# Performance work log

Measured on AMD Instinct MI355X. Metric: run time of the kernel, lower is better.

## Reference

```python
import jax, jax.numpy as jnp
import numpy as np

BF16_MIN = -3.3895313892515355e+38  # torch.finfo(torch.bfloat16).min
B, S, D = 2, 2048, 2048
H, KVH = 32, 8
HD = D // H  # 64


def setup_inputs() -> dict:
    key = jax.random.key(0)
    ks = jax.random.split(key, 7)
    scale = 0.02
    x = jax.random.normal(ks[0], (B, S, D), dtype=jnp.float32)
    # rotary tables as in llama2.c: theta = 10000^{-2i/hd}
    inv_freq = 1.0 / (10000.0 ** (np.arange(0, HD, 2, dtype=np.float32) / HD))
    t = np.arange(S, dtype=np.float32)
    freqs = np.outer(t, inv_freq)  # (S, HD//2)
    freqs_cos = jnp.asarray(np.cos(freqs))
    freqs_sin = jnp.asarray(np.sin(freqs))
    wq = jax.random.normal(ks[1], (H * HD, D), dtype=jnp.float32) * scale
    wk = jax.random.normal(ks[2], (KVH * HD, D), dtype=jnp.float32) * scale
    wv = jax.random.normal(ks[3], (KVH * HD, D), dtype=jnp.float32) * scale
    wo = jax.random.normal(ks[4], (D, H * HD), dtype=jnp.float32) * scale
    attn_mask = jnp.ones((B, S), dtype=jnp.int32)
    return {"x": x, "freqs_cos": freqs_cos, "freqs_sin": freqs_sin,
            "wq": wq, "wk": wk, "wv": wv, "wo": wo, "attn_mask": attn_mask}


def _rope(x, cos, sin):
    # x: (b, s, h, hd) -> split into interleaved real/imag pairs
    b, s, h, hd = x.shape
    xr = x[..., 0::2]
    xi = x[..., 1::2]
    cos = cos[None, :, None, :]  # (1, s, 1, hd//2)
    sin = sin[None, :, None, :]
    out_r = xr * cos - xi * sin
    out_i = xr * sin + xi * cos
    return jnp.stack([out_r, out_i], axis=-1).reshape(b, s, h, hd)


def reference(x, freqs_cos, freqs_sin, wq, wk, wv, wo, attn_mask):
    b, s, d = x.shape
    n_rep = H // KVH
    xq = jnp.einsum('bsd,ed->bse', x, wq).reshape(b, s, H, HD)
    xk = jnp.einsum('bsd,ed->bse', x, wk).reshape(b, s, KVH, HD)
    xv = jnp.einsum('bsd,ed->bse', x, wv).reshape(b, s, KVH, HD)
    xq = _rope(xq, freqs_cos, freqs_sin)
    xk = _rope(xk, freqs_cos, freqs_sin)
    # GQA repeat_kv: (b, s, kvh, hd) -> (b, s, kvh*n_rep, hd)
    xk = jnp.repeat(xk, n_rep, axis=2)
    xv = jnp.repeat(xv, n_rep, axis=2)
    # (b, h, s, hd)
    xq = xq.transpose(0, 2, 1, 3)
    xk = xk.transpose(0, 2, 1, 3)
    xv = xv.transpose(0, 2, 1, 3)
    causal = jnp.triu(jnp.full((s, s), BF16_MIN, dtype=x.dtype), k=1)[None, None]
    pad = jnp.where(attn_mask[:, None, :] == 0, BF16_MIN, 0.0).astype(x.dtype)  # (b,1,s) -> broadcast over query
    combined = causal + pad[:, None, :, :]  # (b,1,s,s)
    scores = jnp.einsum('bhqd,bhkd->bhqk', xq, xk) / np.sqrt(HD).astype(x.dtype)
    scores = jax.nn.softmax(scores + combined, axis=-1)
    out = jnp.einsum('bhqk,bhkd->bhqd', scores, xv)
    out = out.transpose(0, 2, 1, 3).reshape(b, s, H * HD)
    return jnp.einsum('bse,de->bsd', out, wo)
```

## Files before the change

### kernel.cpp

```cpp
#include <hip/hip_runtime.h>

typedef unsigned short u16;
typedef unsigned int u32;
typedef __attribute__((ext_vector_type(8))) short bf16x8;
typedef __attribute__((ext_vector_type(4))) float f32x4;

#define S_LEN 2048
#define QKV_N 3072
#define CEXP 0.18033688011f
#define M32C 5.77078016f

__device__ __forceinline__ u16 f2bf(float f) {
  u32 u = __builtin_bit_cast(u32, f);
  u32 r = (u + 0x7FFFu + ((u >> 16) & 1u)) >> 16;
  return (u16)r;
}
__device__ __forceinline__ float b2f(u16 h) {
  u32 u = ((u32)h) << 16;
  return __builtin_bit_cast(float, u);
}
__device__ __forceinline__ u32 pack_bf(float lo, float hi) {
  u32 a = __builtin_bit_cast(u32, lo) + 0x8000u;
  u32 b = __builtin_bit_cast(u32, hi) + 0x8000u;
  return __builtin_amdgcn_perm(b, a, 0x07060302u);
}
__device__ __forceinline__ void gload16(const void* g, void* l) {
  __builtin_amdgcn_global_load_lds(
      (const __attribute__((address_space(1))) u32*)g,
      (__attribute__((address_space(3))) u32*)l, 16, 0, 0);
}

__global__ void cast_bf16_x4(const float* __restrict__ s, u16* __restrict__ d) {
  int i = blockIdx.x * 256 + threadIdx.x;
  float4 v = ((const float4*)s)[i];
  u32 lo = (u32)f2bf(v.x) | ((u32)f2bf(v.y) << 16);
  u32 hi = (u32)f2bf(v.z) | ((u32)f2bf(v.w) << 16);
  ((uint2*)d)[i] = make_uint2(lo, hi);
}

template <int BN, int WM, int WN, int OUT_BF16>
__global__ __launch_bounds__(512, 2) void gemm_bt2(const u16* __restrict__ A,
                                                   const u16* __restrict__ B,
                                                   void* __restrict__ Cv,
                                                   int K, int ldc, int nbx) {
  constexpr int BM = 256;
  constexpr int MR = BM / WM / 16;
  constexpr int NR = BN / WN / 16;
  constexpr int MR2 = MR / 2, NR2 = NR / 2;
  constexpr int AR = BM / 64, BR = BN / 64;
  __shared__ u16 As0[BM * 64], As1[BM * 64];
  __shared__ u16 Bs0[BN * 64], Bs1[BN * 64];

  const int tid = threadIdx.x;
  const int lane = tid & 63, w = tid >> 6;
  const int wm = w / WN, wn = w % WN;
  const int g = lane >> 4, r16 = lane & 15;
  const int swz = r16 & 7;

  const int nwg = gridDim.x;
  const int q = nwg >> 3, r = nwg & 7;
  const int xcd = blockIdx.x & 7, off = blockIdx.x >> 3;
  const int wg = (xcd < r ? xcd * (q + 1) : r * (q + 1) + (xcd - r) * q) + off;
  const int m0 = (wg / nbx) * BM, n0 = (wg % nbx) * BN;

  const int rowi = tid >> 3;
  const int scol = ((tid & 7) ^ (rowi & 7)) * 8;
  const u16* Ag0 = A + (size_t)(m0 + rowi) * K + scol;
  const u16* Bg0 = B + (size_t)(n0 + rowi) * K + scol;

  f32x4 acc[MR][NR];
#pragma unroll
  for (int mi = 0; mi < MR; ++mi)
#pragma unroll
    for (int ni = 0; ni < NR; ++ni) acc[mi][ni] = f32x4{0.f, 0.f, 0.f, 0.f};

  auto stage = [&](int kb, u16* Ad, u16* Bd) {
#pragma unroll
    for (int rr = 0; rr < AR; ++rr)
      gload16(Ag0 + (size_t)rr * 64 * K + kb, Ad + rr * 4096 + tid * 8);
#pragma unroll
    for (int rr = 0; rr < BR; ++rr)
      gload16(Bg0 + (size_t)rr * 64 * K + kb, Bd + rr * 4096 + tid * 8);
  };

  auto compute = [&](const u16* Asrc, const u16* Bsrc) {
    bf16x8 ac[MR2][2], bc[NR][2];
    const u16* Aw = Asrc + (wm * MR * 16 + r16) * 64;
    const u16* Bw = Bsrc + (wn * NR * 16 + r16) * 64;
#pragma unroll
    for (int mi = 0; mi < MR2; ++mi)
#pragma unroll
      for (int kk = 0; kk < 2; ++kk)
        ac[mi][kk] = *(const bf16x8*)(Aw + mi * 1024 + ((kk * 4 + g) ^ swz) * 8);
#pragma unroll
    for (int ni = 0; ni < NR2; ++ni)
#pragma unroll
      for (int kk = 0; kk < 2; ++kk)
        bc[ni][kk] = *(const bf16x8*)(Bw + ni * 1024 + ((kk * 4 + g) ^ swz) * 8);
    __builtin_amdgcn_s_setprio(1);
#pragma unroll
    for (int mi = 0; mi < MR2; ++mi)
#pragma unroll
      for (int ni = 0; ni < NR2; ++ni)
#pragma unroll
        for (int kk = 0; kk < 2; ++kk)
          acc[mi][ni] = __builtin_amdgcn_mfma_f32_16x16x32_bf16(
              ac[mi][kk], bc[ni][kk], acc[mi][ni], 0, 0, 0);
    __builtin_amdgcn_s_setprio(0);
#pragma unroll
    for (int ni = NR2; ni < NR; ++ni)
#pragma unroll
      for (int kk = 0; kk < 2; ++kk)
        bc[ni][kk] = *(const bf16x8*)(Bw + ni * 1024 + ((kk * 4 + g) ^ swz) * 8);
    __builtin_amdgcn_s_setprio(1);
#pragma unroll
    for (int mi = 0; mi < MR2; ++mi)
#pragma unroll
      for (int ni = NR2; ni < NR; ++ni)
#pragma unroll
        for (int kk = 0; kk < 2; ++kk)
          acc[mi][ni] = __builtin_amdgcn_mfma_f32_16x16x32_bf16(
              ac[mi][kk], bc[ni][kk], acc[mi][ni], 0, 0, 0);
    __builtin_amdgcn_s_setprio(0);
#pragma unroll
    for (int mi = 0; mi < MR2; ++mi)
#pragma unroll
      for (int kk = 0; kk < 2; ++kk)
        ac[mi][kk] =
            *(const bf16x8*)(Aw + (MR2 + mi) * 1024 + ((kk * 4 + g) ^ swz) * 8);
    __builtin_amdgcn_s_setprio(1);
#pragma unroll
    for (int mi = 0; mi < MR2; ++mi)
#pragma unroll
      for (int ni = NR2; ni < NR; ++ni)
#pragma unroll
        for (int kk = 0; kk < 2; ++kk)
          acc[MR2 + mi][ni] = __builtin_amdgcn_mfma_f32_16x16x32_bf16(
              ac[mi][kk], bc[ni][kk], acc[MR2 + mi][ni], 0, 0, 0);
    __builtin_amdgcn_s_setprio(0);
    __builtin_amdgcn_s_setprio(1);
#pragma unroll
    for (int mi = 0; mi < MR2; ++mi)
#pragma unroll
      for (int ni = 0; ni < NR2; ++ni)
#pragma unroll
        for (int kk = 0; kk < 2; ++kk)
          acc[MR2 + mi][ni] = __builtin_amdgcn_mfma_f32_16x16x32_bf16(
              ac[mi][kk], bc[ni][kk], acc[MR2 + mi][ni], 0, 0, 0);
    __builtin_amdgcn_s_setprio(0);
  };

  const int NT = K >> 6;
  stage(0, As0, Bs0);
  __syncthreads();
  for (int t = 0; t < NT; t += 2) {
    if (t + 1 < NT) stage((t + 1) * 64, As1, Bs1);
    compute(As0, Bs0);
    __syncthreads();
    if (t + 2 < NT) stage((t + 2) * 64, As0, Bs0);
    compute(As1, Bs1);
    __syncthreads();
  }

#pragma unroll
  for (int mi = 0; mi < MR; ++mi)
#pragma unroll
    for (int ni = 0; ni < NR; ++ni) {
      int row = m0 + wm * MR * 16 + mi * 16 + g * 4;
      int col = n0 + wn * NR * 16 + ni * 16 + r16;
#pragma unroll
      for (int j = 0; j < 4; ++j) {
        if (OUT_BF16)
          ((u16*)Cv)[(size_t)(row + j) * ldc + col] = f2bf(acc[mi][ni][j]);
        else
          ((float*)Cv)[(size_t)(row + j) * ldc + col] = acc[mi][ni][j];
      }
    }
}

__global__ void rope_k(u16* qkv, const float* __restrict__ fc,
                       const float* __restrict__ fs) {
  const int p = blockIdx.x * 256 + threadIdx.x;
  const int row = blockIdx.y;
  const int s = row & (S_LEN - 1);
  const int i = p & 31;
  const float c = fc[s * 32 + i], sn = fs[s * 32 + i];
  u32 v = *(const u32*)&qkv[(size_t)row * QKV_N + 2 * p];
  float xr = b2f((u16)(v & 0xffffu)), xi = b2f((u16)(v >> 16));
  float orr = xr * c - xi * sn;
  float oi = xr * sn + xi * c;
  u32 o = (u32)f2bf(orr) | ((u32)f2bf(oi) << 16);
  *(u32*)&qkv[(size_t)row * QKV_N + 2 * p] = o;
}

__global__ void vtrans_k(const u16* __restrict__ qkv, u16* __restrict__ vt) {
  int i = blockIdx.x * 256 + threadIdx.x;
  int s = i & 2047;
  int d = (i >> 11) & 63;
  int bk = i >> 17;
  int b = bk >> 3, kv = bk & 7;
  vt[i] = qkv[(size_t)(b * 2048 + s) * QKV_N + 2560 + kv * 64 + d];
}

__global__ __launch_bounds__(256, 3) void attn_fwd(const u16* __restrict__ qkv,
                                                   const u16* __restrict__ vt,
                                                   u16* __restrict__ aout) {
  __shared__ u16 Ks[2][64 * 64];
  __shared__ u16 Vs[2][64 * 64];
  __shared__ u16 Ps[4][16 * 64];

  const int bh = blockIdx.x;
  const int qt = 15 - (int)blockIdx.y;
  const int b = bh >> 5, h = bh & 31, kvh = h >> 2;
  const int tid = threadIdx.x;
  const int w = tid >> 6, lane = tid & 63;
  const int g = lane >> 4, r16 = lane & 15;
  const int q0w = qt * 128 + w * 32;

  const u16* kbase = qkv + (size_t)b * S_LEN * QKV_N + 2048 + kvh * 64;
  const u16* vbase = vt + (size_t)(b * 8 + kvh) * 64 * S_LEN;

  const int srow = lane >> 3;
  const int scol = ((lane & 7) * 8) ^ (srow * 8);
  const int swz = (r16 & 7) * 8;

  bf16x8 qf[2][2];
#pragma unroll
  for (int qs = 0; qs < 2; ++qs) {
    const u16* qrow =
        qkv + (size_t)(b * S_LEN + q0w + qs * 16 + r16) * QKV_N + h * 64;
#pragma unroll
    for (int dh = 0; dh < 2; ++dh)
      qf[qs][dh] = *(const bf16x8*)(qrow + dh * 32 + g * 8);
  }

  f32x4 oacc[2][4];
#pragma unroll
  for (int qs = 0; qs < 2; ++qs)
#pragma unroll
    for (int dt = 0; dt < 4; ++dt) oacc[qs][dt] = f32x4{0.f, 0.f, 0.f, 0.f};
  float lsum[2] = {0.f, 0.f};

  const int nt = qt * 2 + 2;
  const int ntw = ((q0w + 31) >> 6) + 1;

#pragma unroll
  for (int c2 = 0; c2 < 2; ++c2) {
    int c = w * 2 + c2;
    gload16(kbase + (size_t)(c * 8 + srow) * QKV_N + scol, &Ks[0][c * 512]);
    gload16(vbase + (size_t)(c * 8 + srow) * 2048 + scol, &Vs[0][c * 512]);
  }
  __syncthreads();

  int cur = 0;
  for (int t = 0; t < nt; ++t) {
    if (t + 1 < nt) {
      int kk0 = (t + 1) * 64;
#pragma unroll
      for (int c2 = 0; c2 < 2; ++c2) {
        int c = w * 2 + c2;
        gload16(kbase + (size_t)(kk0 + c * 8 + srow) * QKV_N + scol,
                &Ks[cur ^ 1][c * 512]);
        gload16(vbase + (size_t)(c * 8 + srow) * 2048 + kk0 + scol,
                &Vs[cur ^ 1][c * 512]);
      }
    }
    if (t < ntw) {
      const int k0 = t * 64;
      bf16x8 kf[4][2];
#pragma unroll
      for (int ks = 0; ks < 4; ++ks)
#pragma unroll
        for (int dh = 0; dh < 2; ++dh)
          kf[ks][dh] = *(const bf16x8*)&Ks[cur][(ks * 16 + r16) * 64 +
                                               ((dh * 32 + g * 8) ^ swz)];
      bf16x8 vfc[2][4];
#pragma unroll
      for (int ks2 = 0; ks2 < 2; ++ks2)
#pragma unroll
        for (int dt = 0; dt < 4; ++dt)
          vfc[ks2][dt] = *(const bf16x8*)&Vs[cur][(dt * 16 + r16) * 64 +
                                                  ((ks2 * 32 + g * 8) ^ swz)];
      const bool needmask = (k0 + 63 > q0w);
#pragma unroll
      for (int qs = 0; qs < 2; ++qs) {
        f32x4 st[4];
        __builtin_amdgcn_s_setprio(1);
#pragma unroll
        for (int ks = 0; ks < 4; ++ks) {
          f32x4 a = f32x4{0.f, 0.f, 0.f, 0.f};
          a = __builtin_amdgcn_mfma_f32_16x16x32_bf16(kf[ks][0], qf[qs][0], a, 0, 0, 0);
          a = __builtin_amdgcn_mfma_f32_16x16x32_bf16(kf[ks][1], qf[qs][1], a, 0, 0, 0);
          st[ks] = a;
        }
        __builtin_amdgcn_s_setprio(0);
        const int qg = q0w + qs * 16 + r16;
        if (needmask) {
#pragma unroll
          for (int ks = 0; ks < 4; ++ks)
#pragma unroll
            for (int j = 0; j < 4; ++j)
              if (k0 + ks * 16 + g * 4 + j > qg) st[ks][j] = -__builtin_inff();
        }
        float ps = 0.f;
#pragma unroll
        for (int ks = 0; ks < 4; ++ks) {
          float p0 = exp2f(fmaf(st[ks][0], CEXP, -M32C));
          float p1 = exp2f(fmaf(st[ks][1], CEXP, -M32C));
          float p2 = exp2f(fmaf(st[ks][2], CEXP, -M32C));
          float p3 = exp2f(fmaf(st[ks][3], CEXP, -M32C));
          ps += (p0 + p1) + (p2 + p3);
          *(uint2*)&Ps[w][r16 * 64 + ((ks * 16 + g * 4) ^ swz)] =
              make_uint2(pack_bf(p0, p1), pack_bf(p2, p3));
        }
        lsum[qs] += ps;
        __builtin_amdgcn_s_setprio(1);
#pragma unroll
        for (int ks2 = 0; ks2 < 2; ++ks2) {
          bf16x8 pf =
              *(const bf16x8*)&Ps[w][r16 * 64 + ((ks2 * 32 + g * 8) ^ swz)];
#pragma unroll
          for (int dt = 0; dt < 4; ++dt)
            oacc[qs][dt] = __builtin_amdgcn_mfma_f32_16x16x32_bf16(
                pf, vfc[ks2][dt], oacc[qs][dt], 0, 0, 0);
        }
        __builtin_amdgcn_s_setprio(0);
      }
    }
    __syncthreads();
    cur ^= 1;
  }

#pragma unroll
  for (int qs = 0; qs < 2; ++qs) {
    float l = lsum[qs];
    l += __shfl_xor(l, 16);
    l += __shfl_xor(l, 32);
    float inv = 1.f / l;
    float iv[4];
#pragma unroll
    for (int j = 0; j < 4; ++j) iv[j] = __shfl(inv, g * 4 + j);
#pragma unroll
    for (int dt = 0; dt < 4; ++dt)
#pragma unroll
      for (int j = 0; j < 4; ++j) {
        size_t o = (size_t)(b * S_LEN + q0w + qs * 16 + g * 4 + j) * 2048 +
                   h * 64 + dt * 16 + r16;
        aout[o] = f2bf(oacc[qs][dt][j] * iv[j]);
      }
  }
}

extern "C" void kernel_launch(void* const* d_in, const int* in_sizes, int n_in,
                              void* d_out, int out_size, void* d_ws,
                              size_t ws_size, hipStream_t stream) {
  const float* x = (const float*)d_in[0];
  const float* fc = (const float*)d_in[1];
  const float* fs = (const float*)d_in[2];
  const float* wq = (const float*)d_in[3];
  const float* wk = (const float*)d_in[4];
  const float* wv = (const float*)d_in[5];
  const float* wo = (const float*)d_in[6];
  float* out = (float*)d_out;

  char* ws = (char*)d_ws;
  u16* xb = (u16*)(ws);
  u16* wqkvb = (u16*)(ws + 16777216);
  u16* wob = (u16*)(ws + 29360128);
  u16* qkvb = (u16*)(ws + 37748736);
  u16* vtb = (u16*)(ws + 62914560);
  u16* aoutb = (u16*)(ws + 67108864);

  cast_bf16_x4<<<8192, 256, 0, stream>>>(x, xb);
  cast_bf16_x4<<<4096, 256, 0, stream>>>(wq, wqkvb);
  cast_bf16_x4<<<1024, 256, 0, stream>>>(wk, wqkvb + 2048 * 2048);
  cast_bf16_x4<<<1024, 256, 0, stream>>>(wv, wqkvb + 2048 * 2048 + 512 * 2048);
  cast_bf16_x4<<<4096, 256, 0, stream>>>(wo, wob);

  gemm_bt2<256, 2, 4, 1><<<192, 512, 0, stream>>>(xb, wqkvb, qkvb, 2048, 3072, 12);
  rope_k<<<dim3(5, 4096), 256, 0, stream>>>(qkvb, fc, fs);
  vtrans_k<<<8192, 256, 0, stream>>>(qkvb, vtb);
  attn_fwd<<<dim3(64, 16), 256, 0, stream>>>(qkvb, vtb, aoutb);
  gemm_bt2<128, 4, 2, 0><<<256, 512, 0, stream>>>(aoutb, wob, out, 2048, 2048, 16);
}
```

Measured before the change: 199.3 us.

## Fuse bf16 casts into one kernel, use hardware bf16 pack, reorder attention tiles

Replaces the five separate fp32-to-bf16 cast launches with a single kernel that picks its source and destination by index range. Swaps the software bf16 rounding and packing for the v_cvt_pk_bf16_f32 instruction in the cast, RoPE and attention P-packing paths. Changes the query-tile order in attention from strictly heaviest-first to an interleaved heavy/light pattern across blockIdx.y to balance causal work. This removes launch overhead and some ALU work, but the new tile order may change how work is spread across CUs, and the hardware conversion's rounding may differ slightly from the old round-half-up pack.

```diff
diff --git a/kernel.cpp b/kernel.cpp
--- a/kernel.cpp
+++ b/kernel.cpp
@@ -19,10 +19,10 @@
   u32 u = ((u32)h) << 16;
   return __builtin_bit_cast(float, u);
 }
-__device__ __forceinline__ u32 pack_bf(float lo, float hi) {
-  u32 a = __builtin_bit_cast(u32, lo) + 0x8000u;
-  u32 b = __builtin_bit_cast(u32, hi) + 0x8000u;
-  return __builtin_amdgcn_perm(b, a, 0x07060302u);
+__device__ __forceinline__ u32 cvtpk(float lo, float hi) {
+  u32 r;
+  asm("v_cvt_pk_bf16_f32 %0, %1, %2" : "=v"(r) : "v"(lo), "v"(hi));
+  return r;
 }
 __device__ __forceinline__ void gload16(const void* g, void* l) {
   __builtin_amdgcn_global_load_lds(
@@ -30,12 +30,27 @@
       (__attribute__((address_space(3))) u32*)l, 16, 0, 0);
 }
 
-__global__ void cast_bf16_x4(const float* __restrict__ s, u16* __restrict__ d) {
+__global__ void cast_all(const float* __restrict__ x, const float* __restrict__ wq,
+                         const float* __restrict__ wk, const float* __restrict__ wv,
+                         const float* __restrict__ wo, u16* __restrict__ xb,
+                         u16* __restrict__ wqkvb, u16* __restrict__ wob) {
   int i = blockIdx.x * 256 + threadIdx.x;
-  float4 v = ((const float4*)s)[i];
-  u32 lo = (u32)f2bf(v.x) | ((u32)f2bf(v.y) << 16);
-  u32 hi = (u32)f2bf(v.z) | ((u32)f2bf(v.w) << 16);
-  ((uint2*)d)[i] = make_uint2(lo, hi);
+  const float* s;
+  u16* d;
+  int so, dofs;
+  if (i < 2097152) {
+    s = x; d = xb; so = i; dofs = i;
+  } else if (i < 3145728) {
+    s = wq; d = wqkvb; so = i - 2097152; dofs = so;
+  } else if (i < 3407872) {
+    s = wk; d = wqkvb; so = i - 3145728; dofs = so + 1048576;
+  } else if (i < 3670016) {
+    s = wv; d = wqkvb; so = i - 3407872; dofs = so + 1310720;
+  } else {
+    s = wo; d = wob; so = i - 3670016; dofs = so;
+  }
+  float4 v = ((const float4*)s)[so];
+  ((uint2*)d)[dofs] = make_uint2(cvtpk(v.x, v.y), cvtpk(v.z, v.w));
 }
 
 template <int BN, int WM, int WN, int OUT_BF16>
@@ -189,8 +204,7 @@
   float xr = b2f((u16)(v & 0xffffu)), xi = b2f((u16)(v >> 16));
   float orr = xr * c - xi * sn;
   float oi = xr * sn + xi * c;
-  u32 o = (u32)f2bf(orr) | ((u32)f2bf(oi) << 16);
-  *(u32*)&qkv[(size_t)row * QKV_N + 2 * p] = o;
+  *(u32*)&qkv[(size_t)row * QKV_N + 2 * p] = cvtpk(orr, oi);
 }
 
 __global__ void vtrans_k(const u16* __restrict__ qkv, u16* __restrict__ vt) {
@@ -210,7 +224,8 @@
   __shared__ u16 Ps[4][16 * 64];
 
   const int bh = blockIdx.x;
-  const int qt = 15 - (int)blockIdx.y;
+  const int y = blockIdx.y;
+  const int qt = (y < 4) ? (15 - y) : (y < 8) ? (y - 4) : (y < 12) ? y : (19 - y);
   const int b = bh >> 5, h = bh & 31, kvh = h >> 2;
   const int tid = threadIdx.x;
   const int w = tid >> 6, lane = tid & 63;
@@ -311,7 +326,7 @@
           float p3 = exp2f(fmaf(st[ks][3], CEXP, -M32C));
           ps += (p0 + p1) + (p2 + p3);
           *(uint2*)&Ps[w][r16 * 64 + ((ks * 16 + g * 4) ^ swz)] =
-              make_uint2(pack_bf(p0, p1), pack_bf(p2, p3));
+              make_uint2(cvtpk(p0, p1), cvtpk(p2, p3));
         }
         lsum[qs] += ps;
         __builtin_amdgcn_s_setprio(1);
@@ -371,11 +386,7 @@
   u16* vtb = (u16*)(ws + 62914560);
   u16* aoutb = (u16*)(ws + 67108864);
 
-  cast_bf16_x4<<<8192, 256, 0, stream>>>(x, xb);
-  cast_bf16_x4<<<4096, 256, 0, stream>>>(wq, wqkvb);
-  cast_bf16_x4<<<1024, 256, 0, stream>>>(wk, wqkvb + 2048 * 2048);
-  cast_bf16_x4<<<1024, 256, 0, stream>>>(wv, wqkvb + 2048 * 2048 + 512 * 2048);
-  cast_bf16_x4<<<4096, 256, 0, stream>>>(wo, wob);
+  cast_all<<<18432, 256, 0, stream>>>(x, wq, wk, wv, wo, xb, wqkvb, wob);
 
   gemm_bt2<256, 2, 4, 1><<<192, 512, 0, stream>>>(xb, wqkvb, qkvb, 2048, 3072, 12);
   rope_k<<<dim3(5, 4096), 256, 0, stream>>>(qkvb, fc, fs);
```

After: 191.4 us. 3.9% less time.
